# Performance work log

Measured on AMD Instinct MI355X. Metric: run time of the kernel, lower is better.

Reference implementation:

```python
import jax, jax.numpy as jnp
import numpy as np

QI8 = 127.0      # qint8 symmetric max
QI16 = 32767.0   # qint16 symmetric max
MIN_SUB_OUT = -12.0  # SegmentLUT exp input_range lower bound
EPS = 1e-9


def _fq(x, scale, qmax):
    # fake-quantize with straight-through estimator
    q = jnp.clip(jnp.round(x / scale), -qmax - 1.0, qmax) * scale
    return x + jax.lax.stop_gradient(q - x)


def _fq_auto(x, qmax):
    # symmetric max-abs observer (scale is not differentiated, as in QAT)
    s = jax.lax.stop_gradient(jnp.maximum(jnp.max(jnp.abs(x)), EPS)) / qmax
    return _fq(x, s, qmax)


def setup_inputs() -> dict:
    key = jax.random.key(0)
    # pre-softmax logits, quantized with scale 0.0625 -> int8 range ~[-8, 8]
    x = jax.random.normal(key, (8, 4096, 1024), dtype=jnp.float32) * 2.0
    scale = jnp.ones((1,), dtype=jnp.float32) * 0.0625
    return {"x": x, "scale": scale}


def reference(x, scale):
    dim = 1
    # input fake-quant to qint8 grid with given scale (QuantiSoftmaxFunction.forward)
    xq = _fq(x, scale, QI8)
    # sub: x - max(x, dim), qint16 fake-quant (FloatFunctional.sub with int16 qconfig)
    sub = xq - jnp.max(xq, axis=dim, keepdims=True)  # values in (-inf, 0]
    # SegmentLUT exp: input clipped to [min_sub_out, 0], zero gradient below range
    sub = _fq_auto(jnp.clip(sub, MIN_SUB_OUT, 0.0), QI16)
    e = _fq_auto(jnp.exp(sub), QI16)               # LUT exp, qint16 out
    s = _fq_auto(jnp.sum(e, axis=dim, keepdims=True), QI16)  # qint16 sum
    r = _fq_auto(1.0 / s, QI16)                    # LUT reciprocal, qint16
    out = _fq_auto(e * r, QI8)                     # final mul, qint8 output
    return out
```

## Files before the change

kernel.cpp:

```cpp
#include <hip/hip_runtime.h>
#include <math.h>


typedef float       f4 __attribute__((ext_vector_type(4)));
typedef signed char c4 __attribute__((ext_vector_type(4)));

static constexpr int Bdim = 8;
static constexpr int Jdim = 4096;
static constexpr int Cdim = 1024;
static constexpr int NG   = Bdim * Cdim;

static constexpr int JC1   = 16;
static constexpr int NJC   = Jdim / JC1;
static constexpr int GRID1 = Bdim * NJC;

static constexpr size_t SC_B    = 0;
static constexpr size_t GMV_B   = 1024;
static constexpr size_t SARR_B  = 36864;
static constexpr size_t PMAX_B  = 131072;
static constexpr size_t PMIN_B  = PMAX_B + 2097152;
static constexpr size_t CODES_B = 8388608;
static constexpr size_t WS_FULL = CODES_B + 33554432;
static constexpr size_t WS_MIN  = PMIN_B + 2097152;

__device__ __forceinline__ float code8f(float x, float sinv) {
    return fminf(fmaxf(rintf(x * sinv), -128.0f), 127.0f);
}
__device__ __forceinline__ float eq_from(float xq, float gmv, float ssub_inv, float ssub) {
    float sub = fminf(fmaxf(xq - gmv, -12.0f), 0.0f);
    float q   = rintf(sub * ssub_inv);
    float e   = __expf(q * ssub);
    return rintf(e * 32767.0f) * (1.0f / 32767.0f);
}
__device__ __forceinline__ f4 shfl_xor4(f4 v, int off) {
    f4 r; r[0] = __shfl_xor(v[0], off); r[1] = __shfl_xor(v[1], off);
    r[2] = __shfl_xor(v[2], off); r[3] = __shfl_xor(v[3], off); return r;
}
__device__ __forceinline__ f4 fmax4v(f4 a, f4 b) {
    f4 r; r[0]=fmaxf(a[0],b[0]); r[1]=fmaxf(a[1],b[1]);
    r[2]=fmaxf(a[2],b[2]); r[3]=fmaxf(a[3],b[3]); return r;
}
__device__ __forceinline__ f4 fmin4v(f4 a, f4 b) {
    f4 r; r[0]=fminf(a[0],b[0]); r[1]=fminf(a[1],b[1]);
    r[2]=fminf(a[2],b[2]); r[3]=fminf(a[3],b[3]); return r;
}
__device__ __forceinline__ f4 add4v(f4 a, f4 b) {
    f4 r; r[0]=a[0]+b[0]; r[1]=a[1]+b[1]; r[2]=a[2]+b[2]; r[3]=a[3]+b[3]; return r;
}

template <bool WC>
__global__ __launch_bounds__(256) void k_p1(const float* __restrict__ x,
                                            const float* __restrict__ scale,
                                            char* __restrict__ ws) {
    float* sc = (float*)(ws + SC_B);
    if (blockIdx.x == 0 && threadIdx.x == 0) {
        sc[0] = 0.0f;
        sc[1] = 0.0f;
        sc[2] = __int_as_float(0x7f800000);
    }
    const int b  = blockIdx.x / NJC;
    const int jc = blockIdx.x % NJC;
    const int c0 = threadIdx.x * 4;
    const float sinv = 1.0f / scale[0];
    const size_t base = ((size_t)(b * Jdim + jc * JC1)) * Cdim + c0;
    signed char* codes = (signed char*)(ws + CODES_B);

    f4 vmax = {-1e30f, -1e30f, -1e30f, -1e30f};
    f4 vmin = { 1e30f,  1e30f,  1e30f,  1e30f};
#pragma unroll
    for (int r0 = 0; r0 < JC1; r0 += 8) {
        f4 v[8];
#pragma unroll
        for (int j = 0; j < 8; ++j)
            v[j] = __builtin_nontemporal_load(
                reinterpret_cast<const f4*>(x + base + (size_t)(r0 + j) * Cdim));
#pragma unroll
        for (int j = 0; j < 8; ++j) {
            f4 q;
            q[0] = code8f(v[j][0], sinv); q[1] = code8f(v[j][1], sinv);
            q[2] = code8f(v[j][2], sinv); q[3] = code8f(v[j][3], sinv);
            vmax = fmax4v(vmax, q); vmin = fmin4v(vmin, q);
            if (WC)
                *reinterpret_cast<c4*>(codes + base + (size_t)(r0 + j) * Cdim) =
                    (c4){(signed char)(int)q[0], (signed char)(int)q[1],
                         (signed char)(int)q[2], (signed char)(int)q[3]};
        }
    }
    const size_t pidx = (size_t)jc * NG + b * Cdim + c0;
    *reinterpret_cast<c4*>(ws + PMAX_B + pidx) =
        (c4){(signed char)(int)vmax[0], (signed char)(int)vmax[1],
             (signed char)(int)vmax[2], (signed char)(int)vmax[3]};
    *reinterpret_cast<c4*>(ws + PMIN_B + pidx) =
        (c4){(signed char)(int)vmin[0], (signed char)(int)vmin[1],
             (signed char)(int)vmin[2], (signed char)(int)vmin[3]};
}

__global__ __launch_bounds__(256) void k_r1(const float* __restrict__ scale,
                                            char* __restrict__ ws) {
    const signed char* pmax8 = (const signed char*)(ws + PMAX_B);
    const signed char* pmin8 = (const signed char*)(ws + PMIN_B);
    float* gmv = (float*)(ws + GMV_B);
    float* sc  = (float*)(ws + SC_B);

    const int ci  = threadIdx.x & 31;
    const int sub = threadIdx.x >> 5;
    const int g   = blockIdx.x * 32 + ci;

    int mx = -128, mn = 127;
    for (int jc = sub; jc < NJC; jc += 8) {
        const size_t idx = (size_t)jc * NG + g;
        mx = max(mx, (int)pmax8[idx]);
        mn = min(mn, (int)pmin8[idx]);
    }
    __shared__ int smx[8][32], smn[8][32];
    smx[sub][ci] = mx; smn[sub][ci] = mn;
    __syncthreads();
    for (int off = 4; off; off >>= 1) {
        if (sub < off) {
            smx[sub][ci] = max(smx[sub][ci], smx[sub + off][ci]);
            smn[sub][ci] = min(smn[sub][ci], smn[sub + off][ci]);
        }
        __syncthreads();
    }
    __shared__ float sd[32];
    if (sub == 0) {
        const float s = scale[0];
        gmv[g] = (float)smx[0][ci];
        sd[ci] = fminf(12.0f, (float)smx[0][ci] * s - (float)smn[0][ci] * s);
    }
    __syncthreads();
    if (threadIdx.x == 0) {
        float m = sd[0];
#pragma unroll
        for (int i = 1; i < 32; ++i) m = fmaxf(m, sd[i]);
        atomicMax(reinterpret_cast<unsigned int*>(sc + 0), __float_as_uint(m));
    }
}

template <bool UC>
__global__ __launch_bounds__(512) void k_p2(const float* __restrict__ x,
                                            const float* __restrict__ scale,
                                            char* __restrict__ ws) {
    const int g0 = blockIdx.x * 16;
    const int b  = g0 >> 10;
    const int cb = g0 & 1023;
    const int t  = threadIdx.x;
    const int cq = t & 3;
    const int rs = t >> 2;
    const int w  = t >> 6;
    const int l  = t & 63;

    const float s = scale[0];
    const float sinv = 1.0f / s;
    float* sc   = (float*)(ws + SC_B);
    float* gmv  = (float*)(ws + GMV_B);
    float* sarr = (float*)(ws + SARR_B);
    const signed char* codes = (const signed char*)(ws + CODES_B);

    const float amax = fmaxf(sc[0], 1e-9f);
    const float ssub = amax / 32767.0f;
    const float ssub_inv = 1.0f / ssub;
    const f4 gmc = *reinterpret_cast<const f4*>(gmv + g0 + cq * 4);
    const f4 gm  = {gmc[0] * s, gmc[1] * s, gmc[2] * s, gmc[3] * s};

    const size_t base = ((size_t)(b * Jdim + rs)) * Cdim + (size_t)(cb + cq * 4);

    f4 acc = {0.f, 0.f, 0.f, 0.f};
#pragma unroll 8
    for (int k = 0; k < 32; ++k) {
        float xq0, xq1, xq2, xq3;
        if (UC) {
            const c4 q = *reinterpret_cast<const c4*>(codes + base + (size_t)k * 128 * Cdim);
            xq0 = (float)q[0] * s; xq1 = (float)q[1] * s;
            xq2 = (float)q[2] * s; xq3 = (float)q[3] * s;
        } else {
            const f4 v = *reinterpret_cast<const f4*>(x + base + (size_t)k * 128 * Cdim);
            xq0 = code8f(v[0], sinv) * s; xq1 = code8f(v[1], sinv) * s;
            xq2 = code8f(v[2], sinv) * s; xq3 = code8f(v[3], sinv) * s;
        }
        acc[0] += eq_from(xq0, gm[0], ssub_inv, ssub);
        acc[1] += eq_from(xq1, gm[1], ssub_inv, ssub);
        acc[2] += eq_from(xq2, gm[2], ssub_inv, ssub);
        acc[3] += eq_from(xq3, gm[3], ssub_inv, ssub);
    }
#pragma unroll
    for (int off = 4; off < 64; off <<= 1) acc = add4v(acc, shfl_xor4(acc, off));

    __shared__ f4 lA[8][4];
    __shared__ float smx8[8], smn8[8];
    if (l < 4) lA[w][l] = acc;
    __syncthreads();
    if (w == 0 && l < 32) {
        const int wi = l >> 2, cg = l & 3;
        f4 tsum = lA[wi][cg];
#pragma unroll
        for (int off = 4; off < 32; off <<= 1) tsum = add4v(tsum, shfl_xor4(tsum, off));
        if (l < 4) {
            *reinterpret_cast<f4*>(sarr + g0 + l * 4) = tsum;
            float mx = fmaxf(fmaxf(tsum[0], tsum[1]), fmaxf(tsum[2], tsum[3]));
            float mn = fminf(fminf(tsum[0], tsum[1]), fminf(tsum[2], tsum[3]));
            mx = fmaxf(mx, __shfl_xor(mx, 1)); mn = fminf(mn, __shfl_xor(mn, 1));
            mx = fmaxf(mx, __shfl_xor(mx, 2)); mn = fminf(mn, __shfl_xor(mn, 2));
            if (l == 0) { smx8[0] = mx; smn8[0] = mn; }
        }
    }
    __syncthreads();
    if (t == 0) {
        atomicMax(reinterpret_cast<unsigned int*>(sc + 1), __float_as_uint(smx8[0]));
        atomicMin(reinterpret_cast<unsigned int*>(sc + 2), __float_as_uint(smn8[0]));
    }
}

template <bool UC>
__global__ __launch_bounds__(256) void k_p3(const float* __restrict__ x,
                                            const float* __restrict__ scale,
                                            const char* __restrict__ ws,
                                            float* __restrict__ out) {
    const int b  = blockIdx.x / NJC;
    const int jc = blockIdx.x % NJC;
    const int c0 = threadIdx.x * 4;
    const float s = scale[0];
    const float sinv = 1.0f / s;
    const float* sc   = (const float*)(ws + SC_B);
    const float* gmv  = (const float*)(ws + GMV_B);
    const float* sarr = (const float*)(ws + SARR_B);
    const signed char* codes = (const signed char*)(ws + CODES_B);

    const float amax = fmaxf(sc[0], 1e-9f);
    const float ssub = amax / 32767.0f;
    const float ssub_inv = 1.0f / ssub;

    const float max_s = sc[1];
    const float min_s = sc[2];
    const float scale_s = fmaxf(max_s, 1e-9f) / 32767.0f;
    const float ss_inv  = 1.0f / scale_s;
    const float minsq   = fminf(fmaxf(rintf(min_s * ss_inv), -32768.0f), 32767.0f) * scale_s;
    const float maxr    = 1.0f / minsq;
    const float scale_r = fmaxf(maxr, 1e-9f) / 32767.0f;
    const float sr_inv  = 1.0f / scale_r;
    const float maxrq   = fminf(fmaxf(rintf(maxr * sr_inv), -32768.0f), 32767.0f) * scale_r;
    const float scale_out = fmaxf(maxrq, 1e-9f) / 127.0f;
    const float so_inv  = 1.0f / scale_out;

    const f4 gmc = *reinterpret_cast<const f4*>(gmv + b * Cdim + c0);
    const f4 gm  = {gmc[0] * s, gmc[1] * s, gmc[2] * s, gmc[3] * s};
    const f4 s4  = *reinterpret_cast<const f4*>(sarr + b * Cdim + c0);

    f4 rq;
#pragma unroll
    for (int i = 0; i < 4; ++i) {
        float qv = fminf(fmaxf(rintf(s4[i] * ss_inv), -32768.0f), 32767.0f) * scale_s;
        rq[i] = fminf(fmaxf(rintf((1.0f / qv) * sr_inv), -32768.0f), 32767.0f) * scale_r;
    }

    const size_t base = ((size_t)(b * Jdim + jc * JC1)) * Cdim + c0;
#pragma unroll
    for (int r0 = 0; r0 < JC1; r0 += 8) {
        c4 qv[8];
        f4 xv[8];
#pragma unroll
        for (int j = 0; j < 8; ++j) {
            if (UC)
                qv[j] = *reinterpret_cast<const c4*>(codes + base + (size_t)(r0 + j) * Cdim);
            else
                xv[j] = *reinterpret_cast<const f4*>(x + base + (size_t)(r0 + j) * Cdim);
        }
#pragma unroll
        for (int j = 0; j < 8; ++j) {
            float xq0, xq1, xq2, xq3;
            if (UC) {
                xq0 = (float)qv[j][0] * s; xq1 = (float)qv[j][1] * s;
                xq2 = (float)qv[j][2] * s; xq3 = (float)qv[j][3] * s;
            } else {
                xq0 = code8f(xv[j][0], sinv) * s; xq1 = code8f(xv[j][1], sinv) * s;
                xq2 = code8f(xv[j][2], sinv) * s; xq3 = code8f(xv[j][3], sinv) * s;
            }
            const float e0 = eq_from(xq0, gm[0], ssub_inv, ssub) * rq[0];
            const float e1 = eq_from(xq1, gm[1], ssub_inv, ssub) * rq[1];
            const float e2 = eq_from(xq2, gm[2], ssub_inv, ssub) * rq[2];
            const float e3 = eq_from(xq3, gm[3], ssub_inv, ssub) * rq[3];
            f4 o;
            o[0] = fminf(fmaxf(rintf(e0 * so_inv), -128.0f), 127.0f) * scale_out;
            o[1] = fminf(fmaxf(rintf(e1 * so_inv), -128.0f), 127.0f) * scale_out;
            o[2] = fminf(fmaxf(rintf(e2 * so_inv), -128.0f), 127.0f) * scale_out;
            o[3] = fminf(fmaxf(rintf(e3 * so_inv), -128.0f), 127.0f) * scale_out;
            __builtin_nontemporal_store(o,
                reinterpret_cast<f4*>(out + base + (size_t)(r0 + j) * Cdim));
        }
    }
}

extern "C" void kernel_launch(void* const* d_in, const int* in_sizes, int n_in,
                              void* d_out, int out_size, void* d_ws, size_t ws_size,
                              hipStream_t stream) {
    const float* x     = (const float*)d_in[0];
    const float* scale = (const float*)d_in[1];
    float* out = (float*)d_out;
    char* ws   = (char*)d_ws;

    if (ws_size >= WS_FULL) {
        k_p1<true ><<<GRID1, 256, 0, stream>>>(x, scale, ws);
        k_r1<<<NG / 32, 256, 0, stream>>>(scale, ws);
        k_p2<true ><<<NG / 16, 512, 0, stream>>>(x, scale, ws);
        k_p3<true ><<<GRID1, 256, 0, stream>>>(x, scale, ws, out);
    } else {
        k_p1<false><<<GRID1, 256, 0, stream>>>(x, scale, ws);
        k_r1<<<NG / 32, 256, 0, stream>>>(scale, ws);
        k_p2<false><<<NG / 16, 512, 0, stream>>>(x, scale, ws);
        k_p3<false><<<GRID1, 256, 0, stream>>>(x, scale, ws, out);
    }
}
```

Measured before the change: 112.7 us.

## Split column-sum pass into chunked partial sums plus a separate reduction kernel

The exp-sum pass is reorganised to use the same row-chunk grid as the other passes. Each block now writes per-chunk partial sums to workspace, and a new reduction kernel combines them and updates the global max/min atomics, replacing the old in-block shuffle and LDS reduction over strided rows. The aim is a more coalesced access pattern with more blocks, at the cost of an extra launch, extra partial-sum traffic and a larger workspace requirement. The workspace offsets are reorganised to fit the new buffers.

Result: faster. 98.47 us (-12.6%).

```diff
diff --git a/kernel.cpp b/kernel.cpp
--- a/kernel.cpp
+++ b/kernel.cpp
@@ -10,18 +10,18 @@
 static constexpr int Cdim = 1024;
 static constexpr int NG   = Bdim * Cdim;
 
-static constexpr int JC1   = 16;
-static constexpr int NJC   = Jdim / JC1;
+static constexpr int JC    = 16;
+static constexpr int NJC   = Jdim / JC;
 static constexpr int GRID1 = Bdim * NJC;
 
 static constexpr size_t SC_B    = 0;
-static constexpr size_t GMV_B   = 1024;
-static constexpr size_t SARR_B  = 36864;
+static constexpr size_t GMV_B   = 4096;
+static constexpr size_t SARR_B  = GMV_B + (size_t)NG * 4;
 static constexpr size_t PMAX_B  = 131072;
-static constexpr size_t PMIN_B  = PMAX_B + 2097152;
-static constexpr size_t CODES_B = 8388608;
-static constexpr size_t WS_FULL = CODES_B + 33554432;
-static constexpr size_t WS_MIN  = PMIN_B + 2097152;
+static constexpr size_t PMIN_B  = PMAX_B + (size_t)NJC * NG;
+static constexpr size_t PSUM_B  = PMIN_B + (size_t)NJC * NG;
+static constexpr size_t CODES_B = PSUM_B + (size_t)NJC * NG * 4;
+static constexpr size_t WS_NEED = CODES_B + (size_t)Bdim * Jdim * Cdim;
 
 __device__ __forceinline__ float code8f(float x, float sinv) {
     return fminf(fmaxf(rintf(x * sinv), -128.0f), 127.0f);
@@ -32,10 +32,6 @@
     float e   = __expf(q * ssub);
     return rintf(e * 32767.0f) * (1.0f / 32767.0f);
 }
-__device__ __forceinline__ f4 shfl_xor4(f4 v, int off) {
-    f4 r; r[0] = __shfl_xor(v[0], off); r[1] = __shfl_xor(v[1], off);
-    r[2] = __shfl_xor(v[2], off); r[3] = __shfl_xor(v[3], off); return r;
-}
 __device__ __forceinline__ f4 fmax4v(f4 a, f4 b) {
     f4 r; r[0]=fmaxf(a[0],b[0]); r[1]=fmaxf(a[1],b[1]);
     r[2]=fmaxf(a[2],b[2]); r[3]=fmaxf(a[3],b[3]); return r;
@@ -43,9 +39,6 @@
 __device__ __forceinline__ f4 fmin4v(f4 a, f4 b) {
     f4 r; r[0]=fminf(a[0],b[0]); r[1]=fminf(a[1],b[1]);
     r[2]=fminf(a[2],b[2]); r[3]=fminf(a[3],b[3]); return r;
-}
-__device__ __forceinline__ f4 add4v(f4 a, f4 b) {
-    f4 r; r[0]=a[0]+b[0]; r[1]=a[1]+b[1]; r[2]=a[2]+b[2]; r[3]=a[3]+b[3]; return r;
 }
 
 template <bool WC>
@@ -62,13 +55,13 @@
     const int jc = blockIdx.x % NJC;
     const int c0 = threadIdx.x * 4;
     const float sinv = 1.0f / scale[0];
-    const size_t base = ((size_t)(b * Jdim + jc * JC1)) * Cdim + c0;
+    const size_t base = ((size_t)(b * Jdim + jc * JC)) * Cdim + c0;
     signed char* codes = (signed char*)(ws + CODES_B);
 
     f4 vmax = {-1e30f, -1e30f, -1e30f, -1e30f};
     f4 vmin = { 1e30f,  1e30f,  1e30f,  1e30f};
 #pragma unroll
-    for (int r0 = 0; r0 < JC1; r0 += 8) {
+    for (int r0 = 0; r0 < JC; r0 += 8) {
         f4 v[8];
 #pragma unroll
         for (int j = 0; j < 8; ++j)
@@ -138,76 +131,89 @@
 }
 
 template <bool UC>
-__global__ __launch_bounds__(512) void k_p2(const float* __restrict__ x,
+__global__ __launch_bounds__(256) void k_p2(const float* __restrict__ x,
                                             const float* __restrict__ scale,
                                             char* __restrict__ ws) {
-    const int g0 = blockIdx.x * 16;
-    const int b  = g0 >> 10;
-    const int cb = g0 & 1023;
-    const int t  = threadIdx.x;
-    const int cq = t & 3;
-    const int rs = t >> 2;
-    const int w  = t >> 6;
-    const int l  = t & 63;
-
+    const int b  = blockIdx.x / NJC;
+    const int jc = blockIdx.x % NJC;
+    const int c0 = threadIdx.x * 4;
     const float s = scale[0];
     const float sinv = 1.0f / s;
-    float* sc   = (float*)(ws + SC_B);
-    float* gmv  = (float*)(ws + GMV_B);
-    float* sarr = (float*)(ws + SARR_B);
+    const float* sc  = (const float*)(ws + SC_B);
+    const float* gmv = (const float*)(ws + GMV_B);
+    float* psum = (float*)(ws + PSUM_B);
     const signed char* codes = (const signed char*)(ws + CODES_B);
 
     const float amax = fmaxf(sc[0], 1e-9f);
     const float ssub = amax / 32767.0f;
     const float ssub_inv = 1.0f / ssub;
-    const f4 gmc = *reinterpret_cast<const f4*>(gmv + g0 + cq * 4);
+    const f4 gmc = *reinterpret_cast<const f4*>(gmv + b * Cdim + c0);
     const f4 gm  = {gmc[0] * s, gmc[1] * s, gmc[2] * s, gmc[3] * s};
-
-    const size_t base = ((size_t)(b * Jdim + rs)) * Cdim + (size_t)(cb + cq * 4);
+    const size_t base = ((size_t)(b * Jdim + jc * JC)) * Cdim + c0;
 
     f4 acc = {0.f, 0.f, 0.f, 0.f};
-#pragma unroll 8
-    for (int k = 0; k < 32; ++k) {
-        float xq0, xq1, xq2, xq3;
-        if (UC) {
-            const c4 q = *reinterpret_cast<const c4*>(codes + base + (size_t)k * 128 * Cdim);
-            xq0 = (float)q[0] * s; xq1 = (float)q[1] * s;
-            xq2 = (float)q[2] * s; xq3 = (float)q[3] * s;
-        } else {
-            const f4 v = *reinterpret_cast<const f4*>(x + base + (size_t)k * 128 * Cdim);
-            xq0 = code8f(v[0], sinv) * s; xq1 = code8f(v[1], sinv) * s;
-            xq2 = code8f(v[2], sinv) * s; xq3 = code8f(v[3], sinv) * s;
-        }
-        acc[0] += eq_from(xq0, gm[0], ssub_inv, ssub);
-        acc[1] += eq_from(xq1, gm[1], ssub_inv, ssub);
-        acc[2] += eq_from(xq2, gm[2], ssub_inv, ssub);
-        acc[3] += eq_from(xq3, gm[3], ssub_inv, ssub);
-    }
-#pragma unroll
-    for (int off = 4; off < 64; off <<= 1) acc = add4v(acc, shfl_xor4(acc, off));
-
-    __shared__ f4 lA[8][4];
-    __shared__ float smx8[8], smn8[8];
-    if (l < 4) lA[w][l] = acc;
+#pragma unroll
+    for (int r0 = 0; r0 < JC; r0 += 8) {
+        c4 qv[8];
+        f4 xv[8];
+#pragma unroll
+        for (int j = 0; j < 8; ++j) {
+            if (UC)
+                qv[j] = *reinterpret_cast<const c4*>(codes + base + (size_t)(r0 + j) * Cdim);
+            else
+                xv[j] = *reinterpret_cast<const f4*>(x + base + (size_t)(r0 + j) * Cdim);
+        }
+#pragma unroll
+        for (int j = 0; j < 8; ++j) {
+            float xq0, xq1, xq2, xq3;
+            if (UC) {
+                xq0 = (float)qv[j][0] * s; xq1 = (float)qv[j][1] * s;
+                xq2 = (float)qv[j][2] * s; xq3 = (float)qv[j][3] * s;
+            } else {
+                xq0 = code8f(xv[j][0], sinv) * s; xq1 = code8f(xv[j][1], sinv) * s;
+                xq2 = code8f(xv[j][2], sinv) * s; xq3 = code8f(xv[j][3], sinv) * s;
+            }
+            acc[0] += eq_from(xq0, gm[0], ssub_inv, ssub);
+            acc[1] += eq_from(xq1, gm[1], ssub_inv, ssub);
+            acc[2] += eq_from(xq2, gm[2], ssub_inv, ssub);
+            acc[3] += eq_from(xq3, gm[3], ssub_inv, ssub);
+        }
+    }
+    *reinterpret_cast<f4*>(psum + (size_t)jc * NG + b * Cdim + c0) = acc;
+}
+
+__global__ __launch_bounds__(256) void k_r2(char* __restrict__ ws) {
+    const float* psum = (const float*)(ws + PSUM_B);
+    float* sarr = (float*)(ws + SARR_B);
+    float* sc   = (float*)(ws + SC_B);
+
+    const int ci  = threadIdx.x & 31;
+    const int sub = threadIdx.x >> 5;
+    const int g   = blockIdx.x * 32 + ci;
+
+    float p = 0.0f;
+    for (int ch = sub; ch < NJC; ch += 8)
+        p += psum[(size_t)ch * NG + g];
+    __shared__ float sp[8][32];
+    sp[sub][ci] = p;
     __syncthreads();
-    if (w == 0 && l < 32) {
-        const int wi = l >> 2, cg = l & 3;
-        f4 tsum = lA[wi][cg];
-#pragma unroll
-        for (int off = 4; off < 32; off <<= 1) tsum = add4v(tsum, shfl_xor4(tsum, off));
-        if (l < 4) {
-            *reinterpret_cast<f4*>(sarr + g0 + l * 4) = tsum;
-            float mx = fmaxf(fmaxf(tsum[0], tsum[1]), fmaxf(tsum[2], tsum[3]));
-            float mn = fminf(fminf(tsum[0], tsum[1]), fminf(tsum[2], tsum[3]));
-            mx = fmaxf(mx, __shfl_xor(mx, 1)); mn = fminf(mn, __shfl_xor(mn, 1));
-            mx = fmaxf(mx, __shfl_xor(mx, 2)); mn = fminf(mn, __shfl_xor(mn, 2));
-            if (l == 0) { smx8[0] = mx; smn8[0] = mn; }
-        }
+    for (int off = 4; off; off >>= 1) {
+        if (sub < off) sp[sub][ci] += sp[sub + off][ci];
+        __syncthreads();
+    }
+    __shared__ float smx[32], smn[32];
+    if (sub == 0) {
+        const float tv = sp[0][ci];
+        sarr[g] = tv;
+        smx[ci] = tv; smn[ci] = tv;
     }
     __syncthreads();
-    if (t == 0) {
-        atomicMax(reinterpret_cast<unsigned int*>(sc + 1), __float_as_uint(smx8[0]));
-        atomicMin(reinterpret_cast<unsigned int*>(sc + 2), __float_as_uint(smn8[0]));
+    if (threadIdx.x == 0) {
+        float mx = smx[0], mn = smn[0];
+#pragma unroll
+        for (int i = 1; i < 32; ++i) { mx = fmaxf(mx, smx[i]); mn = fminf(mn, smn[i]); }
+        atomicMax(reinterpret_cast<unsigned int*>(sc + 1), __float_as_uint(mx));
+        atomicMin(reinterpret_cast<unsigned int*>(sc + 2), __float_as_uint(mn));
     }
 }
 
@@ -253,9 +259,9 @@
         rq[i] = fminf(fmaxf(rintf((1.0f / qv) * sr_inv), -32768.0f), 32767.0f) * scale_r;
     }
 
-    const size_t base = ((size_t)(b * Jdim + jc * JC1)) * Cdim + c0;
-#pragma unroll
-    for (int r0 = 0; r0 < JC1; r0 += 8) {
+    const size_t base = ((size_t)(b * Jdim + jc * JC)) * Cdim + c0;
+#pragma unroll
+    for (int r0 = 0; r0 < JC; r0 += 8) {
         c4 qv[8];
         f4 xv[8];
 #pragma unroll
@@ -298,15 +304,17 @@
     float* out = (float*)d_out;
     char* ws   = (char*)d_ws;
 
-    if (ws_size >= WS_FULL) {
+    if (ws_size >= WS_NEED) {
         k_p1<true ><<<GRID1, 256, 0, stream>>>(x, scale, ws);
         k_r1<<<NG / 32, 256, 0, stream>>>(scale, ws);
-        k_p2<true ><<<NG / 16, 512, 0, stream>>>(x, scale, ws);
+        k_p2<true ><<<GRID1, 256, 0, stream>>>(x, scale, ws);
+        k_r2<<<NG / 32, 256, 0, stream>>>(ws);
         k_p3<true ><<<GRID1, 256, 0, stream>>>(x, scale, ws, out);
     } else {
         k_p1<false><<<GRID1, 256, 0, stream>>>(x, scale, ws);
         k_r1<<<NG / 32, 256, 0, stream>>>(scale, ws);
-        k_p2<false><<<NG / 16, 512, 0, stream>>>(x, scale, ws);
+        k_p2<false><<<GRID1, 256, 0, stream>>>(x, scale, ws);
+        k_r2<<<NG / 32, 256, 0, stream>>>(ws);
         k_p3<false><<<GRID1, 256, 0, stream>>>(x, scale, ws, out);
     }
 }
```
